# Kernel tuning notes

Hardware: AMD Instinct MI355X
Metric: run time of the kernel (lower is better)

Reference implementation:

```python
import jax, jax.numpy as jnp
import numpy as np

NOOBJ_LAMBDA = 0.5
COORD_LAMBDA = 5.0


def _cxcywh_to_xyxy(b):
    cx, cy, w, h = b[..., 0], b[..., 1], b[..., 2], b[..., 3]
    return jnp.stack([cx - w / 2, cy - h / 2, cx + w / 2, cy + h / 2], axis=-1)


def _pairwise_iou(a, b):
    # a: [B, N, 4] xyxy (preds), b: [B, M, 4] xyxy (targets) -> [B, N, M]
    lt = jnp.maximum(a[:, :, None, :2], b[:, None, :, :2])
    rb = jnp.minimum(a[:, :, None, 2:], b[:, None, :, 2:])
    wh = jnp.clip(rb - lt, 0.0)
    inter = wh[..., 0] * wh[..., 1]
    area_a = (a[..., 2] - a[..., 0]) * (a[..., 3] - a[..., 1])
    area_b = (b[..., 2] - b[..., 0]) * (b[..., 3] - b[..., 1])
    union = area_a[:, :, None] + area_b[:, None, :] - inter
    return inter / jnp.where(union > 0, union, 1.0)


def setup_inputs() -> dict:
    key = jax.random.key(0)
    kp, kt, km = jax.random.split(key, 3)
    B = 8192
    # positive values so sqrt(w), sqrt(h) is well-defined (as the torch code assumes)
    pred = jax.random.uniform(kp, (B, 7, 7, 30), dtype=jnp.float32, minval=0.05, maxval=1.0)
    target = jax.random.uniform(kt, (B, 7, 7, 30), dtype=jnp.float32, minval=0.05, maxval=1.0)
    # target confidence channel (index 4) is the obj/noobj indicator: 0 or 1
    obj = (jax.random.uniform(km, (B, 7, 7)) < 0.2).astype(jnp.float32)
    target = target.at[..., 4].set(obj)
    return {"pred_tensor": pred, "target_tensor": target}


def reference(pred_tensor, target_tensor):
    B = pred_tensor.shape[0]
    pred = pred_tensor.reshape(B, 49, 30)
    target = target_tensor.reshape(B, 49, 30)

    conf_t = target[..., 4]            # [B,49]
    noobj = conf_t == 0                # [B,49]
    obj = conf_t > 0                   # [B,49]

    # --- no-object confidence loss (channels 4 and 9) ---
    d4 = pred[..., 4] - target[..., 4]
    d9 = pred[..., 9] - target[..., 9]
    noobj_loss = jnp.sum(jnp.where(noobj, d4 * d4 + d9 * d9, 0.0))

    # --- object cells: 2 boxes per cell, padded to all 49 cells with a mask ---
    pb = pred[..., :10].reshape(B, 98, 5)
    tb = target[..., :10].reshape(B, 98, 5)
    box_mask = jnp.repeat(obj, 2, axis=1)  # [B,98]

    p_xyxy = _cxcywh_to_xyxy(pb[..., :4])
    t_xyxy = _cxcywh_to_xyxy(tb[..., :4])
    iou = _pairwise_iou(p_xyxy, t_xyxy)  # [B,98,98]
    pair_mask = box_mask[:, :, None] & box_mask[:, None, :]
    iou = jnp.where(pair_mask, iou, 0.0)
    max_iou = jnp.max(iou, axis=1)       # max over pred boxes, per target box [B,98]
    cmask = (max_iou != 0) & box_mask    # [B,98]

    cm = cmask.astype(pred.dtype)
    # coord (cx,cy) loss
    dxy = pb[..., :2] - tb[..., :2]
    coord_loss_cxcy = jnp.sum(cm * jnp.sum(dxy * dxy, axis=-1))
    # coord (sqrt w, sqrt h) loss
    dwh = jnp.sqrt(pb[..., 2:4]) - jnp.sqrt(tb[..., 2:4])
    coord_loss_wh = jnp.sum(cm * jnp.sum(dwh * dwh, axis=-1))
    # object confidence loss
    dconf = pb[..., 4] - tb[..., 4]
    obj_loss = jnp.sum(cm * dconf * dconf)

    # --- class loss over object cells ---
    dcls = pred[..., 10:] - target[..., 10:]
    cls_loss = jnp.sum(obj.astype(pred.dtype) * jnp.sum(dcls * dcls, axis=-1))

    bsz = jnp.asarray(B, pred.dtype)
    batch_cls_loss = cls_loss / bsz
    batch_obj_loss = (obj_loss + noobj_loss * NOOBJ_LAMBDA) / bsz
    batch_coord_loss = (coord_loss_cxcy + coord_loss_wh) * COORD_LAMBDA / bsz
    batch_loss = batch_cls_loss + batch_obj_loss + batch_coord_loss
    return (batch_loss, batch_cls_loss, batch_obj_loss, batch_coord_loss)
```

## Files before the change

kernel.cpp:

```cpp
#include <hip/hip_runtime.h>

#define CH 30
#define CELLS 49
#define ROWF 1470
#define NPAIR 735
#define NQ4 735
#define WPB 4
#define RPBLK 4
#define HITS 6
#define DEPTH 3

__device__ __forceinline__ float waveReduce(float v) {
    #pragma unroll
    for (int o = 32; o > 0; o >>= 1) v += __shfl_xor(v, o, 64);
    return v;
}

__global__ __launch_bounds__(256, 6) void yolo_main(const float* __restrict__ pred,
                                                    const float* __restrict__ targ,
                                                    float* __restrict__ ws, int B,
                                                    int NB) {
    const int w = threadIdx.x >> 6;
    const int lane = threadIdx.x & 63;
    const int h = w & 1;
    const int g = w >> 1;
    const int r0 = blockIdx.x * RPBLK + g * 2;

    __shared__ float boxRaw[2][2][2][CELLS][10];
    __shared__ float4 boxS[WPB][2 * CELLS];
    __shared__ int clist[WPB][CELLS];
    __shared__ float sred[WPB][3];

    float cls = 0.f, objc = 0.f, coord = 0.f;
    unsigned long long m[2] = {0ull, 0ull};
    int nrows = 0;

    const float* P = pred + (size_t)r0 * ROWF;
    const float* T = targ + (size_t)r0 * ROWF;

    if (r0 < B) {
        nrows = (B - r0) >= 2 ? 2 : 1;

        if (nrows == 2) {
            const float4* P4 = (const float4*)P;
            const float4* T4 = (const float4*)T;

            const int cl = lane < CELLS ? lane : CELLS - 1;
            const float conf0 = T[cl * CH + 4];
            const float conf1 = T[ROWF + cl * CH + 4];

            float4 pv[DEPTH], tv[DEPTH];
            #pragma unroll
            for (int s = 0; s < DEPTH; ++s) {
                const int q = lane + (2 * s + h) * 64;
                const int qc = q < NQ4 ? q : NQ4 - 1;
                pv[s] = P4[qc];
                tv[s] = T4[qc];
            }

            m[0] = __ballot((lane < CELLS) && (conf0 > 0.f));
            m[1] = __ballot((lane < CELLS) && (conf1 > 0.f));

            #pragma unroll
            for (int it = 0; it < HITS; ++it) {
                const int slot = it % DEPTH;
                const float4 pa = pv[slot];
                const float4 ta = tv[slot];
                if (it + DEPTH < HITS) {
                    const int qn = lane + (2 * (it + DEPTH) + h) * 64;
                    const int qc = qn < NQ4 ? qn : NQ4 - 1;
                    pv[slot] = P4[qc];
                    tv[slot] = T4[qc];
                }
                const int qq = lane + (2 * it + h) * 64;
                const bool valid = qq < NQ4;
                #pragma unroll
                for (int k = 0; k < 2; ++k) {
                    const int p = 2 * qq + k;
                    const int row = p >= NPAIR ? 1 : 0;
                    const int pr = p - row * NPAIR;
                    const int cell = (pr * 17477) >> 18;
                    const int ch0 = 2 * (pr - cell * 15);
                    const int bit = (int)((m[row] >> cell) & 1ull);
                    const float wobj = (float)bit;
                    const float px = k ? pa.z : pa.x;
                    const float py = k ? pa.w : pa.y;
                    const float tx = k ? ta.z : ta.x;
                    const float ty = k ? ta.w : ta.y;
                    const float dx = px - tx, dy = py - ty;
                    cls += (valid && ch0 >= 10) ? wobj * (dx * dx + dy * dy) : 0.f;
                    const float nn = (ch0 == 4 ? dx * dx : 0.f)
                                   + (ch0 == 8 ? dy * dy : 0.f);
                    objc += valid ? 0.5f * (1.f - wobj) * nn : 0.f;
                    if (valid && bit && ch0 < 10) {
                        float* dp = &boxRaw[g][0][row][cell][ch0];
                        dp[0] = px; dp[1] = py;
                        float* dt = &boxRaw[g][1][row][cell][ch0];
                        dt[0] = tx; dt[1] = ty;
                    }
                }
            }
        } else if (h == 0) {
            const float2* P2 = (const float2*)P;
            const float2* T2 = (const float2*)T;
            const int cl = lane < CELLS ? lane : CELLS - 1;
            const float conf = T[cl * CH + 4];
            const bool isObj = (lane < CELLS) && (conf > 0.f);
            const unsigned long long mask = __ballot(isObj);
            for (int j = lane; j < NPAIR; j += 64) {
                const float2 pq = P2[j], tq = T2[j];
                const int cell = (j * 17477) >> 18;
                const int ch0 = 2 * (j - cell * 15);
                const float wobj = (float)((mask >> cell) & 1ull);
                const float dx = pq.x - tq.x, dy = pq.y - tq.y;
                cls += (ch0 >= 10) ? wobj * (dx * dx + dy * dy) : 0.f;
                const float nn = (ch0 == 4 ? dx * dx : 0.f)
                               + (ch0 == 8 ? dy * dy : 0.f);
                objc += 0.5f * (1.f - wobj) * nn;
            }
            const int nBox = 2 * __popcll(mask);
            if (nBox) {
                if (isObj) clist[w][__popcll(mask & ((1ull << lane) - 1ull))] = lane;
                for (int e = lane; e < nBox; e += 64) {
                    const int c = clist[w][e >> 1];
                    const float* pb = P + c * CH + (e & 1) * 5;
                    const float cx = pb[0], cy = pb[1], bw = pb[2], bh = pb[3];
                    boxS[w][e] = make_float4(cx - 0.5f * bw, cy - 0.5f * bh,
                                             cx + 0.5f * bw, cy + 0.5f * bh);
                }
                for (int e = lane; e < nBox; e += 64) {
                    const int c = clist[w][e >> 1];
                    const float* tb = T + c * CH + (e & 1) * 5;
                    const float tcx = tb[0], tcy = tb[1], tw = tb[2], th = tb[3];
                    const float tx1 = tcx - 0.5f * tw, ty1 = tcy - 0.5f * th;
                    const float tx2 = tcx + 0.5f * tw, ty2 = tcy + 0.5f * th;
                    const float ta2 = (tx2 - tx1) * (ty2 - ty1);
                    float maxiou = 0.f;
                    for (int i = 0; i < nBox; ++i) {
                        const float4 pb4 = boxS[w][i];
                        const float lx = fmaxf(pb4.x, tx1), ly = fmaxf(pb4.y, ty1);
                        const float rx = fminf(pb4.z, tx2), ry = fminf(pb4.w, ty2);
                        const float iw = fmaxf(rx - lx, 0.f), ih = fmaxf(ry - ly, 0.f);
                        const float inter = iw * ih;
                        const float pa2 = (pb4.z - pb4.x) * (pb4.w - pb4.y);
                        const float un = pa2 + ta2 - inter;
                        const float iou = inter / (un > 0.f ? un : 1.f);
                        maxiou = fmaxf(maxiou, iou);
                    }
                    if (maxiou != 0.f) {
                        const float* pb = P + c * CH + (e & 1) * 5;
                        const float dcx = pb[0] - tcx, dcy = pb[1] - tcy;
                        coord += dcx * dcx + dcy * dcy;
                        const float dw = sqrtf(pb[2]) - sqrtf(tw);
                        const float dh = sqrtf(pb[3]) - sqrtf(th);
                        coord += dw * dw + dh * dh;
                        const float dc = pb[4] - tb[4];
                        objc += dc * dc;
                    }
                }
            }
        }
    }

    __syncthreads();

    if (r0 < B && nrows == 2) {
        const unsigned long long mask = m[h];
        const int nBox = 2 * __popcll(mask);
        if (nBox) {
            const bool isObj = (lane < CELLS) && ((mask >> lane) & 1ull);
            if (isObj) clist[w][__popcll(mask & ((1ull << lane) - 1ull))] = lane;

            for (int e = lane; e < nBox; e += 64) {
                const int c = clist[w][e >> 1];
                const float* pb = &boxRaw[g][0][h][c][(e & 1) * 5];
                const float cx = pb[0], cy = pb[1], bw = pb[2], bh = pb[3];
                boxS[w][e] = make_float4(cx - 0.5f * bw, cy - 0.5f * bh,
                                         cx + 0.5f * bw, cy + 0.5f * bh);
            }

            for (int e = lane; e < nBox; e += 64) {
                const int c = clist[w][e >> 1];
                const float* tb = &boxRaw[g][1][h][c][(e & 1) * 5];
                const float tcx = tb[0], tcy = tb[1], tw = tb[2], th = tb[3];
                const float tx1 = tcx - 0.5f * tw, ty1 = tcy - 0.5f * th;
                const float tx2 = tcx + 0.5f * tw, ty2 = tcy + 0.5f * th;
                const float ta2 = (tx2 - tx1) * (ty2 - ty1);
                float maxiou = 0.f;
                for (int i = 0; i < nBox; ++i) {
                    const float4 pb4 = boxS[w][i];
                    const float lx = fmaxf(pb4.x, tx1), ly = fmaxf(pb4.y, ty1);
                    const float rx = fminf(pb4.z, tx2), ry = fminf(pb4.w, ty2);
                    const float iw = fmaxf(rx - lx, 0.f), ih = fmaxf(ry - ly, 0.f);
                    const float inter = iw * ih;
                    const float pa2 = (pb4.z - pb4.x) * (pb4.w - pb4.y);
                    const float un = pa2 + ta2 - inter;
                    const float iou = inter / (un > 0.f ? un : 1.f);
                    maxiou = fmaxf(maxiou, iou);
                }
                if (maxiou != 0.f) {
                    const float* pb = &boxRaw[g][0][h][c][(e & 1) * 5];
                    const float dcx = pb[0] - tcx, dcy = pb[1] - tcy;
                    coord += dcx * dcx + dcy * dcy;
                    const float dw = sqrtf(pb[2]) - sqrtf(tw);
                    const float dh = sqrtf(pb[3]) - sqrtf(th);
                    coord += dw * dw + dh * dh;
                    const float dc = pb[4] - tb[4];
                    objc += dc * dc;
                }
            }
        }
    }

    cls = waveReduce(cls); objc = waveReduce(objc); coord = waveReduce(coord);
    if (lane == 0) { sred[w][0] = cls; sred[w][1] = objc; sred[w][2] = coord; }
    __syncthreads();
    if (threadIdx.x == 0) {
        float C = 0.f, O = 0.f, X = 0.f;
        #pragma unroll
        for (int k = 0; k < WPB; ++k) { C += sred[k][0]; O += sred[k][1]; X += sred[k][2]; }
        ws[blockIdx.x] = C;
        ws[NB + blockIdx.x] = O;
        ws[2 * NB + blockIdx.x] = X;
    }
}

__global__ __launch_bounds__(1024) void yolo_reduce(const float* __restrict__ ws,
                                                    float* __restrict__ out,
                                                    int NB, float invB) {
    const int tid = threadIdx.x;
    const int w = tid >> 6, lane = tid & 63;
    float c = 0.f, o = 0.f, x = 0.f;
    for (int i = tid; i < NB; i += 1024) {
        c += ws[i];
        o += ws[NB + i];
        x += ws[2 * NB + i];
    }
    c = waveReduce(c); o = waveReduce(o); x = waveReduce(x);
    __shared__ float sred[16][3];
    if (lane == 0) { sred[w][0] = c; sred[w][1] = o; sred[w][2] = x; }
    __syncthreads();
    if (tid == 0) {
        float C = 0.f, O = 0.f, X = 0.f;
        #pragma unroll
        for (int k = 0; k < 16; ++k) { C += sred[k][0]; O += sred[k][1]; X += sred[k][2]; }
        const float bcls = C * invB;
        const float bobj = O * invB;
        const float bcoord = X * 5.0f * invB;
        out[0] = bcls + bobj + bcoord;
        out[1] = bcls;
        out[2] = bobj;
        out[3] = bcoord;
    }
}

extern "C" void kernel_launch(void* const* d_in, const int* in_sizes, int n_in,
                              void* d_out, int out_size, void* d_ws, size_t ws_size,
                              hipStream_t stream) {
    const float* pred = (const float*)d_in[0];
    const float* targ = (const float*)d_in[1];
    float* ws = (float*)d_ws;
    float* out = (float*)d_out;
    const int B = in_sizes[0] / ROWF;
    const int NB = (B + RPBLK - 1) / RPBLK;

    yolo_main<<<NB, 256, 0, stream>>>(pred, targ, ws, B, NB);
    yolo_reduce<<<1, 1024, 0, stream>>>(ws, out, NB, 1.0f / (float)B);
}
```

Before: 135.5 us.

## Fuse final reduction via last-block atomic counter and read boxes from global

Removes the separate reduce kernel launch by having the last block to finish (found through an atomic counter) perform the final reduction, with a memset to reset the counter. Drops the shared-memory boxRaw staging and the block-wide barrier before the IoU phase, so each wave reloads its object-box values directly from global memory (likely L2/L1 hits) and moves straight into IoU work. Also lowers the occupancy hint from 6 to 4 blocks per SM. The costs are an extra memset launch, a serialized tail reduction in one block, and more global loads per object box.

```diff
diff --git a/kernel.cpp b/kernel.cpp
--- a/kernel.cpp
+++ b/kernel.cpp
@@ -16,30 +16,30 @@
     return v;
 }
 
-__global__ __launch_bounds__(256, 6) void yolo_main(const float* __restrict__ pred,
+__global__ __launch_bounds__(256, 4) void yolo_main(const float* __restrict__ pred,
                                                     const float* __restrict__ targ,
-                                                    float* __restrict__ ws, int B,
-                                                    int NB) {
+                                                    float* __restrict__ ws,
+                                                    float* __restrict__ out,
+                                                    unsigned int* __restrict__ cnt,
+                                                    int B, int NB, float invB) {
     const int w = threadIdx.x >> 6;
     const int lane = threadIdx.x & 63;
     const int h = w & 1;
     const int g = w >> 1;
     const int r0 = blockIdx.x * RPBLK + g * 2;
 
-    __shared__ float boxRaw[2][2][2][CELLS][10];
     __shared__ float4 boxS[WPB][2 * CELLS];
     __shared__ int clist[WPB][CELLS];
     __shared__ float sred[WPB][3];
+    __shared__ int lastFlag;
 
     float cls = 0.f, objc = 0.f, coord = 0.f;
-    unsigned long long m[2] = {0ull, 0ull};
-    int nrows = 0;
-
-    const float* P = pred + (size_t)r0 * ROWF;
-    const float* T = targ + (size_t)r0 * ROWF;
 
     if (r0 < B) {
-        nrows = (B - r0) >= 2 ? 2 : 1;
+        const int nrows = (B - r0) >= 2 ? 2 : 1;
+        const float* P = pred + (size_t)r0 * ROWF;
+        const float* T = targ + (size_t)r0 * ROWF;
+        unsigned long long m[2] = {0ull, 0ull};
 
         if (nrows == 2) {
             const float4* P4 = (const float4*)P;
@@ -81,8 +81,7 @@
                     const int pr = p - row * NPAIR;
                     const int cell = (pr * 17477) >> 18;
                     const int ch0 = 2 * (pr - cell * 15);
-                    const int bit = (int)((m[row] >> cell) & 1ull);
-                    const float wobj = (float)bit;
+                    const float wobj = (float)((m[row] >> cell) & 1ull);
                     const float px = k ? pa.z : pa.x;
                     const float py = k ? pa.w : pa.y;
                     const float tx = k ? ta.z : ta.x;
@@ -92,11 +91,53 @@
                     const float nn = (ch0 == 4 ? dx * dx : 0.f)
                                    + (ch0 == 8 ? dy * dy : 0.f);
                     objc += valid ? 0.5f * (1.f - wobj) * nn : 0.f;
-                    if (valid && bit && ch0 < 10) {
-                        float* dp = &boxRaw[g][0][row][cell][ch0];
-                        dp[0] = px; dp[1] = py;
-                        float* dt = &boxRaw[g][1][row][cell][ch0];
-                        dt[0] = tx; dt[1] = ty;
+                }
+            }
+
+            const unsigned long long mask = m[h];
+            const int nBox = 2 * __popcll(mask);
+            if (nBox) {
+                const float* Pr = P + h * ROWF;
+                const float* Tr = T + h * ROWF;
+                const bool isObj = (lane < CELLS) && ((mask >> lane) & 1ull);
+                if (isObj) clist[w][__popcll(mask & ((1ull << lane) - 1ull))] = lane;
+
+                for (int e = lane; e < nBox; e += 64) {
+                    const int c = clist[w][e >> 1];
+                    const float* pb = Pr + c * CH + (e & 1) * 5;
+                    const float cx = pb[0], cy = pb[1], bw = pb[2], bh = pb[3];
+                    boxS[w][e] = make_float4(cx - 0.5f * bw, cy - 0.5f * bh,
+                                             cx + 0.5f * bw, cy + 0.5f * bh);
+                }
+
+                for (int e = lane; e < nBox; e += 64) {
+                    const int c = clist[w][e >> 1];
+                    const float* tb = Tr + c * CH + (e & 1) * 5;
+                    const float tcx = tb[0], tcy = tb[1], tw = tb[2], th = tb[3];
+                    const float tx1 = tcx - 0.5f * tw, ty1 = tcy - 0.5f * th;
+                    const float tx2 = tcx + 0.5f * tw, ty2 = tcy + 0.5f * th;
+                    const float ta2 = (tx2 - tx1) * (ty2 - ty1);
+                    float maxiou = 0.f;
+                    for (int i = 0; i < nBox; ++i) {
+                        const float4 pb4 = boxS[w][i];
+                        const float lx = fmaxf(pb4.x, tx1), ly = fmaxf(pb4.y, ty1);
+                        const float rx = fminf(pb4.z, tx2), ry = fminf(pb4.w, ty2);
+                        const float iw = fmaxf(rx - lx, 0.f), ih = fmaxf(ry - ly, 0.f);
+                        const float inter = iw * ih;
+                        const float pa2 = (pb4.z - pb4.x) * (pb4.w - pb4.y);
+                        const float un = pa2 + ta2 - inter;
+                        const float iou = inter / (un > 0.f ? un : 1.f);
+                        maxiou = fmaxf(maxiou, iou);
+                    }
+                    if (maxiou != 0.f) {
+                        const float* pb = Pr + c * CH + (e & 1) * 5;
+                        const float dcx = pb[0] - tcx, dcy = pb[1] - tcy;
+                        coord += dcx * dcx + dcy * dcy;
+                        const float dw = sqrtf(pb[2]) - sqrtf(tw);
+                        const float dh = sqrtf(pb[3]) - sqrtf(th);
+                        coord += dw * dw + dh * dh;
+                        const float dc = pb[4] - tb[4];
+                        objc += dc * dc;
                     }
                 }
             }
@@ -162,56 +203,6 @@
         }
     }
 
-    __syncthreads();
-
-    if (r0 < B && nrows == 2) {
-        const unsigned long long mask = m[h];
-        const int nBox = 2 * __popcll(mask);
-        if (nBox) {
-            const bool isObj = (lane < CELLS) && ((mask >> lane) & 1ull);
-            if (isObj) clist[w][__popcll(mask & ((1ull << lane) - 1ull))] = lane;
-
-            for (int e = lane; e < nBox; e += 64) {
-                const int c = clist[w][e >> 1];
-                const float* pb = &boxRaw[g][0][h][c][(e & 1) * 5];
-                const float cx = pb[0], cy = pb[1], bw = pb[2], bh = pb[3];
-                boxS[w][e] = make_float4(cx - 0.5f * bw, cy - 0.5f * bh,
-                                         cx + 0.5f * bw, cy + 0.5f * bh);
-            }
-
-            for (int e = lane; e < nBox; e += 64) {
-                const int c = clist[w][e >> 1];
-                const float* tb = &boxRaw[g][1][h][c][(e & 1) * 5];
-                const float tcx = tb[0], tcy = tb[1], tw = tb[2], th = tb[3];
-                const float tx1 = tcx - 0.5f * tw, ty1 = tcy - 0.5f * th;
-                const float tx2 = tcx + 0.5f * tw, ty2 = tcy + 0.5f * th;
-                const float ta2 = (tx2 - tx1) * (ty2 - ty1);
-                float maxiou = 0.f;
-                for (int i = 0; i < nBox; ++i) {
-                    const float4 pb4 = boxS[w][i];
-                    const float lx = fmaxf(pb4.x, tx1), ly = fmaxf(pb4.y, ty1);
-                    const float rx = fminf(pb4.z, tx2), ry = fminf(pb4.w, ty2);
-                    const float iw = fmaxf(rx - lx, 0.f), ih = fmaxf(ry - ly, 0.f);
-                    const float inter = iw * ih;
-                    const float pa2 = (pb4.z - pb4.x) * (pb4.w - pb4.y);
-                    const float un = pa2 + ta2 - inter;
-                    const float iou = inter / (un > 0.f ? un : 1.f);
-                    maxiou = fmaxf(maxiou, iou);
-                }
-                if (maxiou != 0.f) {
-                    const float* pb = &boxRaw[g][0][h][c][(e & 1) * 5];
-                    const float dcx = pb[0] - tcx, dcy = pb[1] - tcy;
-                    coord += dcx * dcx + dcy * dcy;
-                    const float dw = sqrtf(pb[2]) - sqrtf(tw);
-                    const float dh = sqrtf(pb[3]) - sqrtf(th);
-                    coord += dw * dw + dh * dh;
-                    const float dc = pb[4] - tb[4];
-                    objc += dc * dc;
-                }
-            }
-        }
-    }
-
     cls = waveReduce(cls); objc = waveReduce(objc); coord = waveReduce(coord);
     if (lane == 0) { sred[w][0] = cls; sred[w][1] = objc; sred[w][2] = coord; }
     __syncthreads();
@@ -223,27 +214,30 @@
         ws[NB + blockIdx.x] = O;
         ws[2 * NB + blockIdx.x] = X;
     }
-}
-
-__global__ __launch_bounds__(1024) void yolo_reduce(const float* __restrict__ ws,
-                                                    float* __restrict__ out,
-                                                    int NB, float invB) {
-    const int tid = threadIdx.x;
-    const int w = tid >> 6, lane = tid & 63;
+
+    __threadfence();
+    if (threadIdx.x == 0) {
+        const unsigned int old = atomicAdd(cnt, 1u);
+        lastFlag = (old == (unsigned int)(NB - 1));
+    }
+    __syncthreads();
+    if (!lastFlag) return;
+    __threadfence();
+
     float c = 0.f, o = 0.f, x = 0.f;
-    for (int i = tid; i < NB; i += 1024) {
-        c += ws[i];
-        o += ws[NB + i];
-        x += ws[2 * NB + i];
+    for (int i = threadIdx.x; i < NB; i += 256) {
+        c += __hip_atomic_load(&ws[i], __ATOMIC_RELAXED, __HIP_MEMORY_SCOPE_AGENT);
+        o += __hip_atomic_load(&ws[NB + i], __ATOMIC_RELAXED, __HIP_MEMORY_SCOPE_AGENT);
+        x += __hip_atomic_load(&ws[2 * NB + i], __ATOMIC_RELAXED, __HIP_MEMORY_SCOPE_AGENT);
     }
     c = waveReduce(c); o = waveReduce(o); x = waveReduce(x);
-    __shared__ float sred[16][3];
+    __syncthreads();
     if (lane == 0) { sred[w][0] = c; sred[w][1] = o; sred[w][2] = x; }
     __syncthreads();
-    if (tid == 0) {
+    if (threadIdx.x == 0) {
         float C = 0.f, O = 0.f, X = 0.f;
         #pragma unroll
-        for (int k = 0; k < 16; ++k) { C += sred[k][0]; O += sred[k][1]; X += sred[k][2]; }
+        for (int k = 0; k < WPB; ++k) { C += sred[k][0]; O += sred[k][1]; X += sred[k][2]; }
         const float bcls = C * invB;
         const float bobj = O * invB;
         const float bcoord = X * 5.0f * invB;
@@ -263,7 +257,9 @@
     float* out = (float*)d_out;
     const int B = in_sizes[0] / ROWF;
     const int NB = (B + RPBLK - 1) / RPBLK;
-
-    yolo_main<<<NB, 256, 0, stream>>>(pred, targ, ws, B, NB);
-    yolo_reduce<<<1, 1024, 0, stream>>>(ws, out, NB, 1.0f / (float)B);
+    unsigned int* cnt = (unsigned int*)((char*)d_ws + (size_t)3 * NB * sizeof(float));
+
+    hipMemsetAsync(cnt, 0, sizeof(unsigned int), stream);
+    yolo_main<<<NB, 256, 0, stream>>>(pred, targ, ws, out, cnt, B, NB,
+                                      1.0f / (float)B);
 }
```

New measurement: 412.2 us. 3.04x slower.
